# Performance work log

Hardware: AMD Instinct MI355X
Metric: run time of the kernel (lower is better)

Reference implementation:

```python
import jax, jax.numpy as jnp
import numpy as np

N_EMBD = 1024
N_HEADS = 16
HEAD_DIM = N_EMBD // N_HEADS
T = 1024
B = 1
WINDOW = 64
LM_STRIDE = 64


def _build_neigh_idx(T, window, stride, n_heads, seed):
    """Per-head neighbor index [H, T, D], padded with -1.

    Neighbors of i: cycle prev/next (sorted), causal window i-window..i-1,
    landmarks j%stride==0 with j<i, then self; deduped preserving order.
    Matches _build_neighbors_index with a single random cycle per head.
    """
    rng = np.random.default_rng(seed)
    n_land = (T + stride - 1) // stride
    D = 2 + window + n_land + 1  # max_cycle_deg + window + landmarks + self
    out = np.full((n_heads, T, D), -1, dtype=np.int64)
    lands = list(range(0, T, stride))
    for h in range(n_heads):
        perm = rng.permutation(T)
        inv = np.argsort(perm)
        prev = perm[(inv - 1) % T]
        nxt = perm[(inv + 1) % T]
        for i in range(T):
            neigh = sorted({int(prev[i]), int(nxt[i])})
            neigh += list(range(max(0, i - window), i))
            neigh += [j for j in lands if j < i]
            neigh.append(i)
            seen = set()
            ded = []
            for j in neigh:
                if j not in seen:
                    ded.append(j)
                    seen.add(j)
            out[h, i, :len(ded)] = ded
    return out


def setup_inputs() -> dict:
    key = jax.random.key(0)
    k1, k2, k3 = jax.random.split(key, 3)
    scale = 1.0 / np.sqrt(N_EMBD)
    x = jax.random.normal(k1, (B, T, N_EMBD), dtype=jnp.float32)
    Wqkv = jax.random.normal(k2, (N_EMBD, 3 * N_EMBD), dtype=jnp.float32) * scale
    Wout = jax.random.normal(k3, (N_EMBD, N_EMBD), dtype=jnp.float32) * scale
    neigh_idx = jnp.asarray(_build_neigh_idx(T, WINDOW, LM_STRIDE, N_HEADS, seed=0))
    return {"x": x, "Wqkv": Wqkv, "Wout": Wout, "neigh_idx": neigh_idx}


def reference(x, Wqkv, Wout, neigh_idx):
    Bv, Tv, C = x.shape
    H, dh = N_HEADS, HEAD_DIM
    qkv = x @ Wqkv  # [B,T,3C]
    q, k, v = jnp.split(qkv, 3, axis=-1)
    q = q.reshape(Bv, Tv, H, dh).transpose(0, 2, 1, 3)  # [B,H,T,dh]
    k = k.reshape(Bv, Tv, H, dh).transpose(0, 2, 1, 3)
    v = v.reshape(Bv, Tv, H, dh).transpose(0, 2, 1, 3)

    safe = jnp.clip(neigh_idx, 0)  # [H,T,D]
    h_ix = jnp.arange(H)[:, None, None]
    k_g = k[:, h_ix, safe, :]  # [B,H,T,D,dh]
    v_g = v[:, h_ix, safe, :]

    scores = jnp.einsum("bhtd,bhtnd->bhtn", q, k_g) / np.sqrt(dh)
    valid = neigh_idx >= 0
    causal = safe <= jnp.arange(Tv)[None, :, None]
    mask = valid & causal  # [H,T,D]; self always present -> rows non-empty
    scores = jnp.where(mask[None], scores, -jnp.inf)
    w = jax.nn.softmax(scores, axis=-1)  # [B,H,T,D]
    y = jnp.einsum("bhtn,bhtnd->bhtd", w, v_g)  # [B,H,T,dh]
    y = y.transpose(0, 2, 1, 3).reshape(Bv, Tv, C)
    return y @ Wout
```

## Files before the change

kernel.cpp:

```cpp
#include <hip/hip_runtime.h>
#include <math.h>

#define NH 16
#define TT 1024
#define HD 64
#define NE 1024

typedef unsigned int u32;
typedef unsigned short u16;
typedef __bf16 bf16x8 __attribute__((ext_vector_type(8)));
typedef float f32x4 __attribute__((ext_vector_type(4)));

__device__ inline u16 f2bf(float f) {
  u32 u = __builtin_bit_cast(u32, f);
  u32 r = (u + 0x7fffu + ((u >> 16) & 1u)) >> 16;
  return (u16)r;
}
__device__ inline float bf2f(u16 h) {
  return __builtin_bit_cast(float, (u32)h << 16);
}
__device__ inline void gload16(const void* g, void* l) {
  __builtin_amdgcn_global_load_lds((const __attribute__((address_space(1))) void*)g,
                                   (__attribute__((address_space(3))) void*)l, 16, 0, 0);
}
__device__ inline u16 h16(uint4 v, int e) {
  u32 w = ((const u32*)&v)[e >> 1];
  return (e & 1) ? (u16)(w >> 16) : (u16)(w & 0xffffu);
}
__device__ inline void block_bar() {
  asm volatile("" ::: "memory");
  __builtin_amdgcn_s_barrier();
  asm volatile("" ::: "memory");
}

__global__ __launch_bounds__(256) void prep(const float* __restrict__ x,
                                            const float* __restrict__ Wqkv,
                                            const float* __restrict__ Wout,
                                            u16* __restrict__ xb,
                                            u16* __restrict__ WqkvT,
                                            u16* __restrict__ WoutT) {
  __shared__ float tile[64][65];
  const int tid = threadIdx.x;
  const int bx = blockIdx.x;
  if (bx < 1024) {
    int i = bx * 256 + tid;
    float4 f = ((const float4*)x)[i];
    ushort4 o = {f2bf(f.x), f2bf(f.y), f2bf(f.z), f2bf(f.w)};
    ((ushort4*)xb)[i] = o;
    return;
  }
  int b = bx - 1024;
  int nb = b & 63, kb = b >> 6;
  const float* W; u16* WT; int N, n0;
  if (nb < 48) { W = Wqkv; WT = WqkvT; N = 3 * NE; n0 = nb * 64; }
  else         { W = Wout; WT = WoutT; N = NE;     n0 = (nb - 48) * 64; }
  const int k0 = kb * 64;
#pragma unroll
  for (int it = 0; it < 16; ++it) {
    int idx = it * 256 + tid;
    int r = idx >> 6, c = idx & 63;
    tile[r][c] = W[(size_t)(k0 + r) * N + n0 + c];
  }
  __syncthreads();
#pragma unroll
  for (int it = 0; it < 16; ++it) {
    int idx = it * 256 + tid;
    int nn = idx >> 6, kk = idx & 63;
    WT[(size_t)(n0 + nn) * NE + k0 + kk] = f2bf(tile[kk][nn]);
  }
}

template<int R>
__device__ __forceinline__ void stage_rows(const u16* __restrict__ G, int ldk,
                                           u16* L, int tid) {
#pragma unroll
  for (int it = 0; it < R / 32; ++it) {
    int idx = it * 256 + tid;
    int r = idx >> 3, kg = idx & 7;
    gload16(G + (size_t)r * ldk + ((kg ^ (r & 7)) << 3), L + (idx << 3));
  }
}

template<int MODE, int NT, int CPX>
__global__ __launch_bounds__(256) void gemm_direct(const u16* __restrict__ A,
                                                   const u16* __restrict__ Bt,
                                                   void* __restrict__ Cv,
                                                   int M, int N, int K) {
  __shared__ u16 As[2][64 * 64];
  __shared__ u16 Bs[2][NT * 64];
  const int tid = threadIdx.x;
  const int lane = tid & 63;
  const int wv = tid >> 6;
  const int wm = wv >> 1, wn = wv & 1;
  const int bid = blockIdx.x;
  const int xcd = bid & 7, loc = bid >> 3;
  const int row0 = (loc / CPX) * 64;
  const int col0 = (xcd * CPX + loc % CPX) * NT;
  const int nsteps = K >> 6;
  constexpr int NI = NT / 32;
  constexpr int SPW = 2 + NI;

  const u16* Ab = A + (size_t)row0 * K;
  const u16* Bb = Bt + (size_t)col0 * K;

  f32x4 acc[2][NI] = {};

  stage_rows<64>(Ab, K, As[0], tid);
  stage_rows<NT>(Bb, K, Bs[0], tid);
  stage_rows<64>(Ab + 64, K, As[1], tid);
  stage_rows<NT>(Bb + 64, K, Bs[1], tid);

  for (int ks = 0; ks < nsteps; ++ks) {
    if (ks < nsteps - 1) {
      if constexpr (SPW == 4) asm volatile("s_waitcnt vmcnt(4)" ::: "memory");
      else                    asm volatile("s_waitcnt vmcnt(3)" ::: "memory");
    } else {
      asm volatile("s_waitcnt vmcnt(0)" ::: "memory");
    }
    __builtin_amdgcn_sched_barrier(0);
    block_bar();

    const int buf = ks & 1;
#pragma unroll
    for (int half = 0; half < 2; ++half) {
      const int kk = half * 32;
      bf16x8 af[2], bfr[NI];
#pragma unroll
      for (int mi = 0; mi < 2; ++mi) {
        int r = wm * 32 + mi * 16 + (lane & 15);
        int c = (kk >> 3) + (lane >> 4);
        af[mi] = *(const bf16x8*)&As[buf][(r * 8 + (c ^ (r & 7))) * 8];
      }
#pragma unroll
      for (int ni = 0; ni < NI; ++ni) {
        int r = wn * (NT / 2) + ni * 16 + (lane & 15);
        int c = (kk >> 3) + (lane >> 4);
        bfr[ni] = *(const bf16x8*)&Bs[buf][(r * 8 + (c ^ (r & 7))) * 8];
      }
#pragma unroll
      for (int mi = 0; mi < 2; ++mi)
#pragma unroll
        for (int ni = 0; ni < NI; ++ni)
          acc[mi][ni] = __builtin_amdgcn_mfma_f32_16x16x32_bf16(af[mi], bfr[ni], acc[mi][ni], 0, 0, 0);
    }

    block_bar();
    if (ks + 2 < nsteps) {
      stage_rows<64>(Ab + (size_t)(ks + 2) * 64, K, As[buf], tid);
      stage_rows<NT>(Bb + (size_t)(ks + 2) * 64, K, Bs[buf], tid);
    }
  }

  const int rbase = row0 + wm * 32 + (lane >> 4) * 4;
  const int cbase = col0 + wn * (NT / 2) + (lane & 15);
#pragma unroll
  for (int mi = 0; mi < 2; ++mi) {
#pragma unroll
    for (int ni = 0; ni < NI; ++ni) {
      int n = cbase + ni * 16;
#pragma unroll
      for (int r = 0; r < 4; ++r) {
        int t = rbase + mi * 16 + r;
        float val = acc[mi][ni][r];
        if (MODE == 0) {
          ((float*)Cv)[(size_t)t * N + n] = val;
        } else {
          int which = n >> 10, h = (n & 1023) >> 6, d = n & 63;
          ((u16*)Cv)[(size_t)which * (NH * TT * HD) + (size_t)h * (TT * HD) +
                     (size_t)t * HD + d] = f2bf(val);
        }
      }
    }
  }
}

__global__ __launch_bounds__(256) void attn5(const u16* __restrict__ qkv,
                                             const int* __restrict__ nidx,
                                             u16* __restrict__ y, int D) {
  __shared__ __align__(16) u16 Qs[16 * 64];
  __shared__ __align__(16) u16 Ks[128 * 64];
  __shared__ __align__(16) u16 Vt[64 * 128];
  __shared__ int pn_l[32];
  __shared__ int colj[128];
  __shared__ float rinv[16];
  float* S = (float*)Ks;
  u16* P = (u16*)((char*)Ks + 8448);

  const int tid = threadIdx.x;
  const int lane = tid & 63;
  const int wv = tid >> 6;
  const int bid = blockIdx.x;
  const int xcd = bid & 7, loc = bid >> 3;
  const int h = xcd * 2 + (loc & 1);
  const int t0 = (loc >> 1) * 16;

  const u16* qh = qkv + (size_t)h * TT * HD;
  const u16* kh = qkv + (size_t)NH * TT * HD + (size_t)h * TT * HD;
  const u16* vh = qkv + 2 * (size_t)NH * TT * HD + (size_t)h * TT * HD;

  if (tid < 32) pn_l[tid] = nidx[((size_t)h * TT + t0 + (tid >> 1)) * D + (tid & 1)];
  if (tid < 128) {
    int row = tid >> 3, slot = tid & 7, ch = slot ^ (row & 7);
    gload16(qh + (size_t)(t0 + row) * HD + ch * 8, Qs + tid * 8);
  }
  __syncthreads();

  if (tid < 128) {
    int c = tid, j;
    if (c < 80) {
      j = t0 - 64 + c;
      if (j < 0) j = -1;
    } else if (c < 96) {
      j = (c - 80) * 64;
      if (j >= t0 - 64) j = -1;
    } else {
      int s = c - 96;
      j = pn_l[s];
      bool keep = (j < t0 - 64) && ((j & 63) != 0);
      if (keep)
        for (int s2 = 0; s2 < s; ++s2)
          if (pn_l[s2] == j) { keep = false; break; }
      if (!keep) j = -1;
    }
    colj[c] = j;
  }
  __syncthreads();

#pragma unroll
  for (int it = 0; it < 4; ++it) {
    int idx = it * 256 + tid;
    int col = idx >> 3, slot = idx & 7, ch = slot ^ (col & 7);
    int j = colj[col]; if (j < 0) j = 0;
    gload16(kh + (size_t)j * HD + ch * 8, Ks + idx * 8);
  }
  const int d0 = (tid & 7) * 8;
  const int cq = tid >> 3;
  uint4 vreg[4];
#pragma unroll
  for (int it = 0; it < 4; ++it) {
    int col = cq * 4 + it;
    int j = colj[col]; if (j < 0) j = 0;
    vreg[it] = *(const uint4*)(vh + (size_t)j * HD + d0);
  }
  __syncthreads();

  f32x4 sc[2] = {};
  bf16x8 af[2];
#pragma unroll
  for (int half = 0; half < 2; ++half) {
    int row = lane & 15;
    int chunk = 4 * half + (lane >> 4);
    af[half] = *(const bf16x8*)&Qs[(row * 8 + (chunk ^ (row & 7))) * 8];
  }
#pragma unroll
  for (int p = 0; p < 2; ++p) {
    int col = 16 * (2 * wv + p) + (lane & 15);
#pragma unroll
    for (int half = 0; half < 2; ++half) {
      int chunk = 4 * half + (lane >> 4);
      bf16x8 bfv = *(const bf16x8*)&Ks[(col * 8 + (chunk ^ (col & 7))) * 8];
      sc[p] = __builtin_amdgcn_mfma_f32_16x16x32_bf16(af[half], bfv, sc[p], 0, 0, 0);
    }
  }
  __syncthreads();

#pragma unroll
  for (int p = 0; p < 2; ++p) {
    int col = 16 * (2 * wv + p) + (lane & 15);
    int j = colj[col];
#pragma unroll
    for (int r = 0; r < 4; ++r) {
      int row = (lane >> 4) * 4 + r;
      int i = t0 + row;
      int p0 = pn_l[2 * row], p1 = pn_l[2 * row + 1];
      bool m;
      if (col < 80)      m = (j >= 0) && (j <= i) &&
                             ((i - j) <= 64 || (j & 63) == 0 || j == p0 || j == p1);
      else if (col < 96) m = (j >= 0);
      else               m = (j >= 0) && (j == p0 || j == p1);
      S[row * 132 + col] = m ? ((float)sc[p][r]) * 0.125f : -1e30f;
    }
  }
  __syncthreads();

  {
    int row = tid >> 4, q = tid & 15;
    float v[8];
    float mx = -3e38f;
#pragma unroll
    for (int e = 0; e < 8; ++e) {
      v[e] = S[row * 132 + 8 * q + e];
      mx = fmaxf(mx, v[e]);
    }
#pragma unroll
    for (int off = 1; off < 16; off <<= 1) mx = fmaxf(mx, __shfl_xor(mx, off, 64));
    float sum = 0.f;
#pragma unroll
    for (int e = 0; e < 8; ++e) {
      v[e] = __expf(v[e] - mx);
      sum += v[e];
    }
#pragma unroll
    for (int off = 1; off < 16; off <<= 1) sum += __shfl_xor(sum, off, 64);
    if (q == 0) rinv[row] = 1.0f / sum;
    u32 w0 = (u32)f2bf(v[0]) | ((u32)f2bf(v[1]) << 16);
    u32 w1 = (u32)f2bf(v[2]) | ((u32)f2bf(v[3]) << 16);
    u32 w2 = (u32)f2bf(v[4]) | ((u32)f2bf(v[5]) << 16);
    u32 w3 = (u32)f2bf(v[6]) | ((u32)f2bf(v[7]) << 16);
    uint4 pk = {w0, w1, w2, w3};
    *(uint4*)&P[row * 128 + ((q ^ (row & 7)) << 3)] = pk;
  }

#pragma unroll
  for (int e = 0; e < 8; ++e) {
    int d = d0 + e;
    u32 lo = (u32)h16(vreg[0], e) | ((u32)h16(vreg[1], e) << 16);
    u32 hi = (u32)h16(vreg[2], e) | ((u32)h16(vreg[3], e) << 16);
    int oswz = (cq >> 1) ^ (d & 7) ^ ((d >> 3) & 7);
    uint2 pk2 = {lo, hi};
    *(uint2*)&Vt[d * 128 + oswz * 8 + (cq & 1) * 4] = pk2;
  }
  __syncthreads();

  f32x4 oacc = {};
#pragma unroll
  for (int ks2 = 0; ks2 < 4; ++ks2) {
    int rowp = lane & 15;
    int chp = ks2 * 4 + (lane >> 4);
    bf16x8 pa = *(const bf16x8*)&P[rowp * 128 + ((chp ^ (rowp & 7)) << 3)];
    int dd = wv * 16 + (lane & 15);
    int swz = chp ^ (dd & 7) ^ ((dd >> 3) & 7);
    bf16x8 vb = *(const bf16x8*)&Vt[dd * 128 + swz * 8];
    oacc = __builtin_amdgcn_mfma_f32_16x16x32_bf16(pa, vb, oacc, 0, 0, 0);
  }
  {
    int dd = wv * 16 + (lane & 15);
#pragma unroll
    for (int r = 0; r < 4; ++r) {
      int row = (lane >> 4) * 4 + r;
      y[(size_t)(t0 + row) * NE + h * HD + dd] = f2bf(oacc[r] * rinv[row]);
    }
  }
}

extern "C" void kernel_launch(void* const* d_in, const int* in_sizes, int n_in,
                              void* d_out, int out_size, void* d_ws, size_t ws_size,
                              hipStream_t stream) {
  const float* x    = (const float*)d_in[0];
  const float* Wqkv = (const float*)d_in[1];
  const float* Wout = (const float*)d_in[2];
  const int*   nidx = (const int*)d_in[3];
  float* out = (float*)d_out;

  u16* ws16  = (u16*)d_ws;
  u16* xb    = ws16;
  u16* WqkvT = ws16 + 1048576;
  u16* WoutT = ws16 + 4194304;
  u16* qkvb  = ws16 + 5242880;

  const int D = in_sizes[3] / (NH * TT);

  prep<<<2048, 256, 0, stream>>>(x, Wqkv, Wout, xb, WqkvT, WoutT);

  gemm_direct<1, 64, 6><<<768, 256, 0, stream>>>(xb, WqkvT, qkvb, TT, 3 * NE, NE);

  attn5<<<1024, 256, 0, stream>>>(qkvb, nidx, xb, D);

  gemm_direct<0, 32, 4><<<512, 256, 0, stream>>>(xb, WoutT, out, TT, NE, NE);
}
```

Before: 45.79 us.

## Split K across waves in GEMM with LDS reduction of partial accumulators

Reassigns the four waves of each GEMM block so that each wave covers all 64 rows of the output tile but only half of every 64-wide K step. Pairs of waves then add their partial accumulators through LDS scratch in the epilogue. The aim is fewer LDS fragment reads per MFMA, since A fragments are no longer duplicated across the wave grid. The cost is an extra LDS round trip, two block barriers at the end, and stores issued by only half the waves.

New measurement: 46.09 us. No clear change (+0.7%).

```diff
diff --git a/kernel.cpp b/kernel.cpp
--- a/kernel.cpp
+++ b/kernel.cpp
@@ -82,28 +82,31 @@
 }
 
 template<int MODE, int NT, int CPX>
-__global__ __launch_bounds__(256) void gemm_direct(const u16* __restrict__ A,
-                                                   const u16* __restrict__ Bt,
-                                                   void* __restrict__ Cv,
-                                                   int M, int N, int K) {
+__global__ __launch_bounds__(256) void gemm_kh(const u16* __restrict__ A,
+                                               const u16* __restrict__ Bt,
+                                               void* __restrict__ Cv,
+                                               int M, int N, int K) {
   __shared__ u16 As[2][64 * 64];
   __shared__ u16 Bs[2][NT * 64];
   const int tid = threadIdx.x;
   const int lane = tid & 63;
   const int wv = tid >> 6;
-  const int wm = wv >> 1, wn = wv & 1;
+  const int wn = wv & 1;
+  const int kh = wv >> 1;
   const int bid = blockIdx.x;
   const int xcd = bid & 7, loc = bid >> 3;
   const int row0 = (loc / CPX) * 64;
   const int col0 = (xcd * CPX + loc % CPX) * NT;
   const int nsteps = K >> 6;
-  constexpr int NI = NT / 32;
-  constexpr int SPW = 2 + NI;
+  constexpr int NI = NT / 64;
+  static_assert(NT == 64 || NT == 32, "NT");
+  constexpr int NIr = (NT == 64) ? 2 : 1;
+  constexpr int SPW = 2 + NT / 32;
 
   const u16* Ab = A + (size_t)row0 * K;
   const u16* Bb = Bt + (size_t)col0 * K;
 
-  f32x4 acc[2][NI] = {};
+  f32x4 acc[4][NIr] = {};
 
   stage_rows<64>(Ab, K, As[0], tid);
   stage_rows<NT>(Bb, K, Bs[0], tid);
@@ -121,28 +124,23 @@
     block_bar();
 
     const int buf = ks & 1;
-#pragma unroll
-    for (int half = 0; half < 2; ++half) {
-      const int kk = half * 32;
-      bf16x8 af[2], bfr[NI];
-#pragma unroll
-      for (int mi = 0; mi < 2; ++mi) {
-        int r = wm * 32 + mi * 16 + (lane & 15);
-        int c = (kk >> 3) + (lane >> 4);
-        af[mi] = *(const bf16x8*)&As[buf][(r * 8 + (c ^ (r & 7))) * 8];
-      }
-#pragma unroll
-      for (int ni = 0; ni < NI; ++ni) {
-        int r = wn * (NT / 2) + ni * 16 + (lane & 15);
-        int c = (kk >> 3) + (lane >> 4);
-        bfr[ni] = *(const bf16x8*)&Bs[buf][(r * 8 + (c ^ (r & 7))) * 8];
-      }
-#pragma unroll
-      for (int mi = 0; mi < 2; ++mi)
-#pragma unroll
-        for (int ni = 0; ni < NI; ++ni)
-          acc[mi][ni] = __builtin_amdgcn_mfma_f32_16x16x32_bf16(af[mi], bfr[ni], acc[mi][ni], 0, 0, 0);
-    }
+    const int c = kh * 4 + (lane >> 4);
+    bf16x8 af[4], bfr[NIr];
+#pragma unroll
+    for (int mi = 0; mi < 4; ++mi) {
+      int r = mi * 16 + (lane & 15);
+      af[mi] = *(const bf16x8*)&As[buf][(r * 8 + (c ^ (r & 7))) * 8];
+    }
+#pragma unroll
+    for (int ni = 0; ni < NIr; ++ni) {
+      int r = wn * (NT / 2) + ni * 16 + (lane & 15);
+      bfr[ni] = *(const bf16x8*)&Bs[buf][(r * 8 + (c ^ (r & 7))) * 8];
+    }
+#pragma unroll
+    for (int mi = 0; mi < 4; ++mi)
+#pragma unroll
+      for (int ni = 0; ni < NIr; ++ni)
+        acc[mi][ni] = __builtin_amdgcn_mfma_f32_16x16x32_bf16(af[mi], bfr[ni], acc[mi][ni], 0, 0, 0);
 
     block_bar();
     if (ks + 2 < nsteps) {
@@ -151,23 +149,36 @@
     }
   }
 
-  const int rbase = row0 + wm * 32 + (lane >> 4) * 4;
-  const int cbase = col0 + wn * (NT / 2) + (lane & 15);
-#pragma unroll
-  for (int mi = 0; mi < 2; ++mi) {
-#pragma unroll
-    for (int ni = 0; ni < NI; ++ni) {
-      int n = cbase + ni * 16;
-#pragma unroll
-      for (int r = 0; r < 4; ++r) {
-        int t = rbase + mi * 16 + r;
-        float val = acc[mi][ni][r];
-        if (MODE == 0) {
-          ((float*)Cv)[(size_t)t * N + n] = val;
-        } else {
-          int which = n >> 10, h = (n & 1023) >> 6, d = n & 63;
-          ((u16*)Cv)[(size_t)which * (NH * TT * HD) + (size_t)h * (TT * HD) +
-                     (size_t)t * HD + d] = f2bf(val);
+  float* scratch = (float*)&As[0][0];
+  __syncthreads();
+  if (kh == 1) {
+#pragma unroll
+    for (int mi = 0; mi < 4; ++mi)
+#pragma unroll
+      for (int ni = 0; ni < NIr; ++ni)
+        *(f32x4*)&scratch[(((wn * NIr + ni) * 4 + mi) * 64 + lane) * 4] = acc[mi][ni];
+  }
+  __syncthreads();
+  if (kh == 0) {
+    const int cbase = col0 + wn * (NT / 2) + (lane & 15);
+#pragma unroll
+    for (int mi = 0; mi < 4; ++mi) {
+#pragma unroll
+      for (int ni = 0; ni < NIr; ++ni) {
+        f32x4 o = acc[mi][ni] +
+                  *(const f32x4*)&scratch[(((wn * NIr + ni) * 4 + mi) * 64 + lane) * 4];
+        int n = cbase + ni * 16;
+#pragma unroll
+        for (int r = 0; r < 4; ++r) {
+          int t = row0 + mi * 16 + (lane >> 4) * 4 + r;
+          float val = o[r];
+          if (MODE == 0) {
+            ((float*)Cv)[(size_t)t * N + n] = val;
+          } else {
+            int which = n >> 10, h = (n & 1023) >> 6, d = n & 63;
+            ((u16*)Cv)[(size_t)which * (NH * TT * HD) + (size_t)h * (TT * HD) +
+                       (size_t)t * HD + d] = f2bf(val);
+          }
         }
       }
     }
@@ -362,9 +373,9 @@
 
   prep<<<2048, 256, 0, stream>>>(x, Wqkv, Wout, xb, WqkvT, WoutT);
 
-  gemm_direct<1, 64, 6><<<768, 256, 0, stream>>>(xb, WqkvT, qkvb, TT, 3 * NE, NE);
+  gemm_kh<1, 64, 6><<<768, 256, 0, stream>>>(xb, WqkvT, qkvb, TT, 3 * NE, NE);
 
   attn5<<<1024, 256, 0, stream>>>(qkvb, nidx, xb, D);
 
-  gemm_direct<0, 32, 4><<<512, 256, 0, stream>>>(xb, WoutT, out, TT, NE, NE);
-}
+  gemm_kh<0, 32, 4><<<512, 256, 0, stream>>>(xb, WoutT, out, TT, NE, NE);
+}
```
